# Optimization experiments

Hardware: AMD Instinct MI355X
Metric: run time of the kernel (lower is better)

## Reference

```python
import jax, jax.numpy as jnp
import numpy as np

IN_DIM = 128
HIDDEN = 256
OUT_DIM = 128
N_NODES = 100000
N_EDGES = 500000
N_MC = 2


def setup_inputs() -> dict:
    key = jax.random.key(0)
    k1, k2, k3, k4 = jax.random.split(key, 4)
    edge_index = jax.random.randint(k1, (2, N_EDGES), 0, N_NODES, dtype=jnp.int64)
    mc_embeddings = jax.random.normal(k2, (N_MC, N_NODES, IN_DIM), dtype=jnp.float32)
    # kaiming_normal for Linear1 (fan_in = 2*IN_DIM) and Linear2 (fan_in = HIDDEN)
    W1 = jax.random.normal(k3, (2 * IN_DIM, HIDDEN), dtype=jnp.float32) * np.sqrt(2.0 / (2 * IN_DIM))
    b1 = jnp.zeros((HIDDEN,), dtype=jnp.float32)
    W2 = jax.random.normal(k4, (HIDDEN, OUT_DIM), dtype=jnp.float32) * np.sqrt(2.0 / HIDDEN)
    b2 = jnp.zeros((OUT_DIM,), dtype=jnp.float32)
    return {"edge_index": edge_index, "mc_embeddings": mc_embeddings,
            "W1": W1, "b1": b1, "W2": W2, "b2": b2}


def reference(edge_index, mc_embeddings, W1, b1, W2, b2):
    # cat([x[src], x[dst]]) @ W1 == x[src] @ W1[:D] + x[dst] @ W1[D:]
    src, dst = edge_index[0], edge_index[1]
    W1a, W1b = W1[:IN_DIM], W1[IN_DIM:]  # [D, H] each

    def per_mc(x):  # x: [N, D]
        h = x[src] @ W1a + x[dst] @ W1b + b1          # [E, H]
        h = jax.nn.relu(h)
        return h @ W2 + b2                            # [E, out]

    return jax.vmap(per_mc)(mc_embeddings)           # [M, E, out]
```

## Files before the change

### kernel.cpp

```cpp
#include <hip/hip_runtime.h>
#include <hip/hip_bf16.h>

#define IN_DIM   128
#define HIDDEN   256
#define OUT_DIM  128
#define N_NODES  100000
#define N_EDGES  500000
#define N_ROWS   (2 * N_EDGES)

typedef __bf16 bf16x8  __attribute__((ext_vector_type(8)));
typedef float  f32x16  __attribute__((ext_vector_type(16)));

#define W1S_OFF 0
#define W2S_OFF 131072

__global__ void prep_weights(const float* __restrict__ W1,
                             const float* __restrict__ W2,
                             unsigned char* __restrict__ ws) {
  int t = blockIdx.x * 256 + threadIdx.x;
  if (t < HIDDEN * HIDDEN) {
    int n = t & 255, k = t >> 8;
    __bf16 b = (__bf16)W1[k * HIDDEN + n];
    int byte = W1S_OFF + n * 512 + ((k * 2) ^ ((n & 7) << 4));
    *reinterpret_cast<__bf16*>(ws + byte) = b;
  } else {
    int t2 = t - HIDDEN * HIDDEN;
    if (t2 < HIDDEN * OUT_DIM) {
      int n = t2 & 127, k = t2 >> 7;
      __bf16 b = (__bf16)W2[k * OUT_DIM + n];
      int byte = W2S_OFF + n * 512 + ((k * 2) ^ ((n & 7) << 4));
      *reinterpret_cast<__bf16*>(ws + byte) = b;
    }
  }
}

static __device__ __forceinline__ unsigned pack_bf16(float a, float b) {
  __bf16 x = (__bf16)a, y = (__bf16)b;
  unsigned short ux = __builtin_bit_cast(unsigned short, x);
  unsigned short uy = __builtin_bit_cast(unsigned short, y);
  return (unsigned)ux | ((unsigned)uy << 16);
}

__global__ __launch_bounds__(128)
void edge_mlp(const int* __restrict__ eidx,
              const float* __restrict__ x,
              const float* __restrict__ b1,
              const float* __restrict__ b2,
              const unsigned char* __restrict__ ws,
              float* __restrict__ out) {
  __shared__ __align__(16) unsigned char wbuf[16384];

  const int tid  = threadIdx.x;
  const int wv   = tid >> 6;
  const int lane = tid & 63;
  const int el   = lane & 31;
  const int hi   = lane >> 5;

  const long base = (long)blockIdx.x * 64;
  const long gr   = base + wv * 32 + el;
  const int  mc   = (gr >= N_EDGES) ? 1 : 0;
  const int  e    = (int)(gr - (long)mc * N_EDGES);
  const int  sn   = eidx[e];
  const int  dn   = eidx[N_EDGES + e];
  const float* xs = x + ((long)mc * N_NODES + sn) * IN_DIM;
  const float* xd = x + ((long)mc * N_NODES + dn) * IN_DIM;

  bf16x8 a1[16];
#pragma unroll
  for (int s = 0; s < 16; ++s) {
    int k0 = s * 16 + hi * 8;
    const float* p = (s < 8) ? (xs + k0) : (xd + (k0 - IN_DIM));
    float4 f0 = *reinterpret_cast<const float4*>(p);
    float4 f1 = *reinterpret_cast<const float4*>(p + 4);
    bf16x8 a;
    a[0] = (__bf16)f0.x; a[1] = (__bf16)f0.y; a[2] = (__bf16)f0.z; a[3] = (__bf16)f0.w;
    a[4] = (__bf16)f1.x; a[5] = (__bf16)f1.y; a[6] = (__bf16)f1.z; a[7] = (__bf16)f1.w;
    a1[s] = a;
  }

#define STAGE(t)                                                               \
  do {                                                                         \
    const unsigned char* g_ = ws + (t) * 16384;                                \
    _Pragma("unroll")                                                          \
    for (int i_ = 0; i_ < 8; ++i_) {                                           \
      __builtin_amdgcn_global_load_lds(                                        \
          (const __attribute__((address_space(1))) unsigned int*)(g_ + i_ * 2048 + tid * 16), \
          (__attribute__((address_space(3))) unsigned int*)(&wbuf[i_ * 2048 + tid * 16]),     \
          16, 0, 0);                                                           \
    }                                                                          \
  } while (0)

  const int rowb = el * 512;
  const int swz  = (el & 7) << 4;

  bf16x8 a2[16];

#pragma unroll
  for (int cc = 0; cc < 8; ++cc) {
    __syncthreads();
    STAGE(cc);
    __syncthreads();
    f32x16 acc = {};
#pragma unroll
    for (int ks = 0; ks < 16; ++ks) {
      bf16x8 wf = *reinterpret_cast<const bf16x8*>(
          &wbuf[rowb + ((ks * 32 + hi * 16) ^ swz)]);
      acc = __builtin_amdgcn_mfma_f32_32x32x16_bf16(wf, a1[ks], acc, 0, 0, 0);
    }
    float4 bv0 = *reinterpret_cast<const float4*>(b1 + cc * 32 + hi * 4);
    float4 bv1 = *reinterpret_cast<const float4*>(b1 + cc * 32 + 8 + hi * 4);
    float4 bv2 = *reinterpret_cast<const float4*>(b1 + cc * 32 + 16 + hi * 4);
    float4 bv3 = *reinterpret_cast<const float4*>(b1 + cc * 32 + 24 + hi * 4);
    unsigned w0 = pack_bf16(fmaxf(acc[0] + bv0.x, 0.f),  fmaxf(acc[1] + bv0.y, 0.f));
    unsigned w1 = pack_bf16(fmaxf(acc[2] + bv0.z, 0.f),  fmaxf(acc[3] + bv0.w, 0.f));
    unsigned w2 = pack_bf16(fmaxf(acc[4] + bv1.x, 0.f),  fmaxf(acc[5] + bv1.y, 0.f));
    unsigned w3 = pack_bf16(fmaxf(acc[6] + bv1.z, 0.f),  fmaxf(acc[7] + bv1.w, 0.f));
    unsigned w4 = pack_bf16(fmaxf(acc[8] + bv2.x, 0.f),  fmaxf(acc[9] + bv2.y, 0.f));
    unsigned w5 = pack_bf16(fmaxf(acc[10] + bv2.z, 0.f), fmaxf(acc[11] + bv2.w, 0.f));
    unsigned w6 = pack_bf16(fmaxf(acc[12] + bv3.x, 0.f), fmaxf(acc[13] + bv3.y, 0.f));
    unsigned w7 = pack_bf16(fmaxf(acc[14] + bv3.z, 0.f), fmaxf(acc[15] + bv3.w, 0.f));
    asm("v_permlane32_swap_b32 %0, %1" : "+v"(w0), "+v"(w2));
    asm("v_permlane32_swap_b32 %0, %1" : "+v"(w1), "+v"(w3));
    asm("v_permlane32_swap_b32 %0, %1" : "+v"(w4), "+v"(w6));
    asm("v_permlane32_swap_b32 %0, %1" : "+v"(w5), "+v"(w7));
    uint4 fe; fe.x = w0; fe.y = w1; fe.z = w2; fe.w = w3;
    uint4 fo; fo.x = w4; fo.y = w5; fo.z = w6; fo.w = w7;
    a2[2 * cc]     = __builtin_bit_cast(bf16x8, fe);
    a2[2 * cc + 1] = __builtin_bit_cast(bf16x8, fo);
  }

#pragma unroll
  for (int oc = 0; oc < 4; ++oc) {
    __syncthreads();
    STAGE(8 + oc);
    __syncthreads();
    f32x16 acc = {};
#pragma unroll
    for (int kk = 0; kk < 16; ++kk) {
      bf16x8 wf = *reinterpret_cast<const bf16x8*>(
          &wbuf[rowb + ((kk * 32 + hi * 16) ^ swz)]);
      acc = __builtin_amdgcn_mfma_f32_32x32x16_bf16(a2[kk], wf, acc, 0, 0, 0);
    }
    float bvo = b2[oc * 32 + el];
    const long r0 = base + wv * 32;
#pragma unroll
    for (int reg = 0; reg < 16; ++reg) {
      int m = (reg & 3) + 8 * (reg >> 2) + 4 * hi;
      out[(r0 + m) * OUT_DIM + oc * 32 + el] = acc[reg] + bvo;
    }
  }
#undef STAGE
}

extern "C" void kernel_launch(void* const* d_in, const int* in_sizes, int n_in,
                              void* d_out, int out_size, void* d_ws, size_t ws_size,
                              hipStream_t stream) {
  const int*   eidx = (const int*)d_in[0];
  const float* x    = (const float*)d_in[1];
  const float* b1   = (const float*)d_in[3];
  const float* b2   = (const float*)d_in[5];
  float* out = (float*)d_out;
  unsigned char* ws = (unsigned char*)d_ws;

  prep_weights<<<(HIDDEN * HIDDEN + HIDDEN * OUT_DIM) / 256, 256, 0, stream>>>(
      (const float*)d_in[2], (const float*)d_in[4], ws);

  edge_mlp<<<N_ROWS / 64, 128, 0, stream>>>(eidx, x, b1, b2, ws, out);
  (void)in_sizes; (void)n_in; (void)out_size; (void)ws_size;
}
```

Measured before the change: 362.5 us.

## Load weight MFMA fragments directly from global memory instead of staging through LDS

Weights are repacked in the prep kernel into a fragment-major layout so each lane can read its 16-byte MFMA operand with a single coalesced global load. The LDS staging buffer and the pair of __syncthreads around each weight chunk are removed. This eliminates block-wide barriers and LDS traffic, relying on L1/L2 caching of the 192KB weight set shared across all blocks. In exchange, every wave reads weights from cache separately, which adds global/L2 load latency and bandwidth, and those loads must now be hidden inside the MFMA loop.

Measured after the change: 755.7 us. 2.08x slower.

```diff
diff --git a/kernel.cpp b/kernel.cpp
--- a/kernel.cpp
+++ b/kernel.cpp
@@ -11,7 +11,6 @@
 typedef __bf16 bf16x8  __attribute__((ext_vector_type(8)));
 typedef float  f32x16  __attribute__((ext_vector_type(16)));
 
-#define W1S_OFF 0
 #define W2S_OFF 131072
 
 __global__ void prep_weights(const float* __restrict__ W1,
@@ -21,14 +20,16 @@
   if (t < HIDDEN * HIDDEN) {
     int n = t & 255, k = t >> 8;
     __bf16 b = (__bf16)W1[k * HIDDEN + n];
-    int byte = W1S_OFF + n * 512 + ((k * 2) ^ ((n & 7) << 4));
+    int byte = (n >> 5) * 16384 + (k >> 4) * 1024 + ((k >> 3) & 1) * 512
+             + (n & 31) * 16 + (k & 7) * 2;
     *reinterpret_cast<__bf16*>(ws + byte) = b;
   } else {
     int t2 = t - HIDDEN * HIDDEN;
     if (t2 < HIDDEN * OUT_DIM) {
       int n = t2 & 127, k = t2 >> 7;
       __bf16 b = (__bf16)W2[k * OUT_DIM + n];
-      int byte = W2S_OFF + n * 512 + ((k * 2) ^ ((n & 7) << 4));
+      int byte = W2S_OFF + (n >> 5) * 16384 + (k >> 4) * 1024
+               + ((k >> 3) & 1) * 512 + (n & 31) * 16 + (k & 7) * 2;
       *reinterpret_cast<__bf16*>(ws + byte) = b;
     }
   }
@@ -48,8 +49,6 @@
               const float* __restrict__ b2,
               const unsigned char* __restrict__ ws,
               float* __restrict__ out) {
-  __shared__ __align__(16) unsigned char wbuf[16384];
-
   const int tid  = threadIdx.x;
   const int wv   = tid >> 6;
   const int lane = tid & 63;
@@ -78,33 +77,17 @@
     a1[s] = a;
   }
 
-#define STAGE(t)                                                               \
-  do {                                                                         \
-    const unsigned char* g_ = ws + (t) * 16384;                                \
-    _Pragma("unroll")                                                          \
-    for (int i_ = 0; i_ < 8; ++i_) {                                           \
-      __builtin_amdgcn_global_load_lds(                                        \
-          (const __attribute__((address_space(1))) unsigned int*)(g_ + i_ * 2048 + tid * 16), \
-          (__attribute__((address_space(3))) unsigned int*)(&wbuf[i_ * 2048 + tid * 16]),     \
-          16, 0, 0);                                                           \
-    }                                                                          \
-  } while (0)
-
-  const int rowb = el * 512;
-  const int swz  = (el & 7) << 4;
+  const unsigned char* wfrag = ws + hi * 512 + el * 16;
 
   bf16x8 a2[16];
 
 #pragma unroll
   for (int cc = 0; cc < 8; ++cc) {
-    __syncthreads();
-    STAGE(cc);
-    __syncthreads();
+    const unsigned char* wc = wfrag + cc * 16384;
     f32x16 acc = {};
 #pragma unroll
     for (int ks = 0; ks < 16; ++ks) {
-      bf16x8 wf = *reinterpret_cast<const bf16x8*>(
-          &wbuf[rowb + ((ks * 32 + hi * 16) ^ swz)]);
+      bf16x8 wf = *reinterpret_cast<const bf16x8*>(wc + ks * 1024);
       acc = __builtin_amdgcn_mfma_f32_32x32x16_bf16(wf, a1[ks], acc, 0, 0, 0);
     }
     float4 bv0 = *reinterpret_cast<const float4*>(b1 + cc * 32 + hi * 4);
@@ -131,14 +114,11 @@
 
 #pragma unroll
   for (int oc = 0; oc < 4; ++oc) {
-    __syncthreads();
-    STAGE(8 + oc);
-    __syncthreads();
+    const unsigned char* wc = wfrag + W2S_OFF + oc * 16384;
     f32x16 acc = {};
 #pragma unroll
     for (int kk = 0; kk < 16; ++kk) {
-      bf16x8 wf = *reinterpret_cast<const bf16x8*>(
-          &wbuf[rowb + ((kk * 32 + hi * 16) ^ swz)]);
+      bf16x8 wf = *reinterpret_cast<const bf16x8*>(wc + kk * 1024);
       acc = __builtin_amdgcn_mfma_f32_32x32x16_bf16(a2[kk], wf, acc, 0, 0, 0);
     }
     float bvo = b2[oc * 32 + el];
@@ -149,7 +129,6 @@
       out[(r0 + m) * OUT_DIM + oc * 32 + el] = acc[reg] + bvo;
     }
   }
-#undef STAGE
 }
 
 extern "C" void kernel_launch(void* const* d_in, const int* in_sizes, int n_in,
```
